# Performance work log

Measured on AMD Instinct MI355X. Metric: run time of the kernel, lower is better.

Reference implementation:

```python
import jax, jax.numpy as jnp
import numpy as np
import math

N = 2048; L = 100; D_IN = 128; D_STATE = 16; D_INNER = 256
MAMBA_DIM = 128; GAT_HID = 64; HEADS = 4; GAT_OUT = 64


def _lin(key, fin, fout, scale=0.02):
    k1, k2 = jax.random.split(key)
    return (jax.random.normal(k1, (fin, fout), jnp.float32) * scale,
            jnp.zeros((fout,), jnp.float32))


def setup_inputs() -> dict:
    key = jax.random.key(0)
    ks = jax.random.split(key, 16)
    temporal_data = jax.random.normal(ks[0], (N, L, D_IN), jnp.float32)
    graph_x = jax.random.normal(ks[1], (N, D_IN), jnp.float32)
    adj = (jax.random.uniform(ks[2], (N, N)) < 0.005).astype(jnp.float32)
    adj_matrix = jnp.maximum(adj, jnp.eye(N, dtype=jnp.float32))
    pos_emb = jax.random.normal(ks[3], (1, 100, D_IN), jnp.float32)
    Wi, bi = _lin(ks[4], D_IN, D_INNER)
    Wg, bg = _lin(ks[5], D_IN, D_INNER)
    A_log = jnp.linspace(math.log(1e-3), math.log(0.1), D_STATE).reshape(1, D_STATE).astype(jnp.float32)
    Wb, bb = _lin(ks[6], D_INNER, D_STATE)
    Wc, bc = _lin(ks[7], D_IN, D_STATE)
    Wo, bo = _lin(ks[8], D_INNER, D_IN)
    Wfc, bfc = _lin(ks[9], D_IN, MAMBA_DIM)
    W1 = jax.random.normal(ks[10], (HEADS, D_IN, GAT_HID), jnp.float32) * 0.05
    a1 = jax.random.normal(ks[11], (HEADS, 2 * GAT_HID), jnp.float32) * 0.05
    W2 = jax.random.normal(ks[12], (1, HEADS * GAT_HID, GAT_OUT), jnp.float32) * 0.05
    a2 = jax.random.normal(ks[13], (1, 2 * GAT_OUT), jnp.float32) * 0.05
    return dict(temporal_data=temporal_data, graph_x=graph_x, adj_matrix=adj_matrix,
                pos_emb=pos_emb, Wi=Wi, bi=bi, Wg=Wg, bg=bg, A_log=A_log,
                Wb=Wb, bb=bb, Wc=Wc, bc=bc, Wo=Wo, bo=bo, Wfc=Wfc, bfc=bfc,
                W1=W1, a1=a1, W2=W2, a2=a2)


def _mamba(x, pos_emb, Wi, bi, Wg, bg, A_log, Wb, bb, Wc, bc, Wo, bo):
    Bt, Ls, _ = x.shape
    x = x + pos_emb[:, :Ls, :]
    x_gated = (x @ Wi + bi) * jax.nn.sigmoid(x @ Wg + bg)   # [B,L,d_inner]
    Bmat = x_gated @ Wb + bb                                 # [B,L,d_state]
    Cmat = x @ Wc + bc                                       # [B,L,d_state]
    A = jnp.exp(0.01 * jnp.exp(A_log))                       # [1,d_state] (dt=0.01)

    def step(h, bc):
        b, c = bc
        h = A * h + b
        return h, h * c

    h0 = jnp.zeros((Bt, A_log.shape[1]), x.dtype)
    _, ys = jax.lax.scan(step, h0, (jnp.swapaxes(Bmat, 0, 1), jnp.swapaxes(Cmat, 0, 1)))
    y = jnp.swapaxes(ys, 0, 1)                               # [B,L,d_state]
    d_inner = Wo.shape[0]
    out_exp = jnp.concatenate(
        [y, jnp.zeros((Bt, Ls, d_inner - y.shape[-1]), x.dtype)], axis=-1)
    return out_exp @ Wo + bo


def _gat_layer(x, adj, W, a, concat):
    # x: [N,Fin], W: [H,Fin,Fout], a: [H,2*Fout]
    F_out = W.shape[2]
    xt = jnp.einsum('nf,hfo->hno', x, W)                     # [H,N,Fout]
    e_src = jnp.einsum('hno,ho->hn', xt, a[:, :F_out])       # a . x_i part
    e_dst = jnp.einsum('hno,ho->hn', xt, a[:, F_out:])       # a . x_j part
    e = jax.nn.leaky_relu(e_src[:, :, None] + e_dst[:, None, :], 0.2)
    e = jnp.where(adj[None, :, :] > 0, e, -jnp.inf)
    att = jax.nn.softmax(e, axis=2)                          # masked entries -> 0
    h_prime = jnp.einsum('hij,hjo->hio', att, xt)            # [H,N,Fout]
    if concat:
        return jnp.transpose(h_prime, (1, 0, 2)).reshape(x.shape[0], -1)
    return h_prime.mean(axis=0)


def reference(temporal_data, graph_x, adj_matrix, pos_emb, Wi, bi, Wg, bg, A_log,
              Wb, bb, Wc, bc, Wo, bo, Wfc, bfc, W1, a1, W2, a2):
    mamba_out = _mamba(temporal_data, pos_emb, Wi, bi, Wg, bg, A_log, Wb, bb, Wc, bc, Wo, bo)
    mamba_features = mamba_out @ Wfc + bfc
    # GAT stack (dropout is identity in eval mode)
    h = _gat_layer(graph_x, adj_matrix, W1, a1, concat=True)
    h = jax.nn.relu(h)
    gat_features = _gat_layer(h, adj_matrix, W2, a2, concat=False)
    return mamba_features, gat_features
```

## Files before the change

### kernel.cpp

```cpp
#include <hip/hip_runtime.h>
#include <hip/hip_bf16.h>

#define N_NODES 2048
#define L_SEQ   100
#define ROWS    (N_NODES * L_SEQ)
#define HEADS   4
#define GHID    64

typedef __attribute__((ext_vector_type(8))) short bf16x8;
typedef __attribute__((ext_vector_type(4))) float floatx4;

__device__ __forceinline__ short f2bf(float f) {
    union { float f; unsigned u; } v; v.f = f;
    return (short)((v.u + 0x8000u) >> 16);
}

constexpr size_t OFF_WCOMB = 0;
constexpr size_t OFF_BCOMB = 2048;
constexpr size_t OFF_AEXP  = 2176;
constexpr size_t OFF_WIGS  = 2192;
constexpr size_t OFF_WBS   = 34960;
constexpr size_t OFF_WCS   = 37008;
constexpr size_t OFF_BM    = 38032;
constexpr size_t OFF_CM    = OFF_BM + (size_t)ROWS * 16;
constexpr size_t OFF_XT1   = OFF_BM;
constexpr size_t OFF_ES1   = OFF_XT1 + (size_t)HEADS * N_NODES * GHID;
constexpr size_t OFF_ED1   = OFF_ES1 + HEADS * N_NODES;
constexpr size_t OFF_H1    = OFF_ED1 + HEADS * N_NODES;
constexpr size_t OFF_XT2   = OFF_H1 + (size_t)N_NODES * 256;
constexpr size_t OFF_ES2   = OFF_XT2 + (size_t)N_NODES * 64;
constexpr size_t OFF_ED2   = OFF_ES2 + N_NODES;

__global__ __launch_bounds__(256) void kA_prep(
    const float* __restrict__ Wo, const float* __restrict__ bo,
    const float* __restrict__ Wfc, const float* __restrict__ bfc,
    const float* __restrict__ A_log,
    const float* __restrict__ Wi, const float* __restrict__ Wg,
    const float* __restrict__ Wb, const float* __restrict__ Wc,
    float* __restrict__ ws) {
    const int b = blockIdx.x;
    if (b < 9) {
        int i = b * 256 + threadIdx.x;
        if (i < 2048) {
            int row = i >> 7, col = i & 127;
            float a = 0.f;
            for (int f = 0; f < 128; f++) a += Wo[row * 128 + f] * Wfc[f * 128 + col];
            ws[OFF_WCOMB + i] = a;
        } else if (i < 2176) {
            int col = i - 2048;
            float acc = bfc[col];
            for (int f = 0; f < 128; f++) acc += bo[f] * Wfc[f * 128 + col];
            ws[OFF_BCOMB + col] = acc;
        } else if (i < 2192) {
            int s = i - 2176;
            ws[OFF_AEXP + s] = expf(0.01f * expf(A_log[s]));
        }
        return;
    }
    int i = (b - 9) * 256 + threadIdx.x;
    short* wigs = (short*)(ws + OFF_WIGS);
    short* wbs  = (short*)(ws + OFF_WBS);
    short* wcs  = (short*)(ws + OFF_WCS);
    if (i < 65536) {
        int j = i & 7, lane = (i >> 3) & 63, ks = (i >> 9) & 3, nt = i >> 11;
        int w = nt >> 3, t = nt & 7;
        int col = w * 64 + (t & 3) * 16 + (lane & 15);
        int k   = ks * 32 + (lane >> 4) * 8 + j;
        float v = (t < 4) ? Wi[k * 256 + col] : Wg[k * 256 + col];
        wigs[i] = f2bf(v);
    } else if (i < 65536 + 4096) {
        int ii = i - 65536;
        int j = ii & 7, lane = (ii >> 3) & 63, ks = ii >> 9;
        int k = ks * 32 + (lane >> 4) * 8 + j, n = lane & 15;
        wbs[ii] = f2bf(Wb[k * 16 + n]);
    } else if (i < 65536 + 4096 + 2048) {
        int ii = i - 65536 - 4096;
        int j = ii & 7, lane = (ii >> 3) & 63, ks = ii >> 9;
        int k = ks * 32 + (lane >> 4) * 8 + j, n = lane & 15;
        wcs[ii] = f2bf(Wc[k * 16 + n]);
    }
}

__global__ __launch_bounds__(512, 4) void k1_mfma(
    const float* __restrict__ temporal, const float* __restrict__ pos,
    const float* __restrict__ bi, const float* __restrict__ bg,
    const float* __restrict__ bb, const float* __restrict__ bc,
    const float* __restrict__ ws, float* __restrict__ Bm, float* __restrict__ Cm) {
    __shared__ short xbf[64][136];
    __shared__ short gbf[64][264];
    const int tid = threadIdx.x, wave = tid >> 6, lane = tid & 63;
    const int m = lane & 15, quad = lane >> 4;
    const int r0 = blockIdx.x * 64;
    const int l0 = r0 % L_SEQ;

#pragma unroll
    for (int i = 0; i < 4; i++) {
        int f4  = i * 512 + tid;
        int row = f4 >> 5;
        int c4  = (f4 & 31) * 4;
        int l = l0 + row; if (l >= L_SEQ) l -= L_SEQ;
        float4 tv = *(const float4*)(temporal + (size_t)(r0 + row) * 128 + c4);
        float4 pv = *(const float4*)(pos + l * 128 + c4);
        short4 sv;
        sv.x = f2bf(tv.x + pv.x); sv.y = f2bf(tv.y + pv.y);
        sv.z = f2bf(tv.z + pv.z); sv.w = f2bf(tv.w + pv.w);
        *(short4*)&xbf[row][c4] = sv;
    }
    __syncthreads();

    const short* Wigs = (const short*)(ws + OFF_WIGS);
    const int wg = wave >> 1, wp = wave & 1;
    floatx4 acc[4][4] = {};
#pragma unroll
    for (int ks = 0; ks < 4; ks++) {
        bf16x8 bfr[4];
#pragma unroll
        for (int jl = 0; jl < 4; jl++) {
            int ntg = wg * 8 + wp * 2 + (jl & 1) + ((jl >> 1) << 2);
            bfr[jl] = *(const bf16x8*)(Wigs + (size_t)((ntg * 4 + ks) * 64 + lane) * 8);
        }
        bf16x8 afr[4];
#pragma unroll
        for (int mt = 0; mt < 4; mt++)
            afr[mt] = *(const bf16x8*)&xbf[mt * 16 + m][ks * 32 + quad * 8];
#pragma unroll
        for (int mt = 0; mt < 4; mt++)
#pragma unroll
            for (int jl = 0; jl < 4; jl++)
                acc[mt][jl] = __builtin_amdgcn_mfma_f32_16x16x32_bf16(
                    afr[mt], bfr[jl], acc[mt][jl], 0, 0, 0);
    }

    const float NL2E = -1.44269504f;
#pragma unroll
    for (int tp = 0; tp < 2; tp++) {
        int col = wave * 32 + tp * 16 + m;
        float biv = bi[col];
        float bgs = bg[col] * NL2E;
#pragma unroll
        for (int mt = 0; mt < 4; mt++) {
#pragma unroll
            for (int r = 0; r < 4; r++) {
                float li = acc[mt][tp][r] + biv;
                float ex = __builtin_amdgcn_exp2f(fmaf(acc[mt][tp + 2][r], NL2E, bgs));
                float g  = li * __builtin_amdgcn_rcpf(1.f + ex);
                gbf[mt * 16 + quad * 4 + r][col] = f2bf(g);
            }
        }
    }
    __syncthreads();

    if (wave < 4) {
        const short* Wbs = (const short*)(ws + OFF_WBS);
        floatx4 accB = {};
#pragma unroll
        for (int ks = 0; ks < 8; ks++) {
            bf16x8 a = *(const bf16x8*)&gbf[wave * 16 + m][ks * 32 + quad * 8];
            bf16x8 b = *(const bf16x8*)(Wbs + (size_t)(ks * 64 + lane) * 8);
            accB = __builtin_amdgcn_mfma_f32_16x16x32_bf16(a, b, accB, 0, 0, 0);
        }
        float bbv = bb[m];
#pragma unroll
        for (int r = 0; r < 4; r++) {
            int row = r0 + wave * 16 + quad * 4 + r;
            Bm[(size_t)row * 16 + m] = accB[r] + bbv;
        }
    } else {
        const short* Wcs = (const short*)(ws + OFF_WCS);
        const int mt = wave - 4;
        floatx4 accC = {};
#pragma unroll
        for (int ks = 0; ks < 4; ks++) {
            bf16x8 a = *(const bf16x8*)&xbf[mt * 16 + m][ks * 32 + quad * 8];
            bf16x8 b = *(const bf16x8*)(Wcs + (size_t)(ks * 64 + lane) * 8);
            accC = __builtin_amdgcn_mfma_f32_16x16x32_bf16(a, b, accC, 0, 0, 0);
        }
        float bcv = bc[m];
#pragma unroll
        for (int r = 0; r < 4; r++) {
            int row = r0 + mt * 16 + quad * 4 + r;
            Cm[(size_t)row * 16 + m] = accC[r] + bcv;
        }
    }
}

__global__ __launch_bounds__(256) void k2_scan(const float* __restrict__ ws,
                                               float* __restrict__ out) {
    __shared__ float sb[2][1600], sc[2][1600];
    const int sub = threadIdx.x >> 7, f = threadIdx.x & 127;
    const int n = blockIdx.x * 2 + sub;
    const float4* Bm4 = (const float4*)(ws + OFF_BM + (size_t)n * 1600);
    const float4* Cm4 = (const float4*)(ws + OFF_CM + (size_t)n * 1600);
#pragma unroll
    for (int i = 0; i < 4; i++) {
        int idx = i * 128 + f;
        if (idx < 400) {
            ((float4*)sb[sub])[idx] = Bm4[idx];
            ((float4*)sc[sub])[idx] = Cm4[idx];
        }
    }
    float w[16], A[16], h[16];
#pragma unroll
    for (int s = 0; s < 16; s++) {
        w[s] = ws[OFF_WCOMB + s * 128 + f];
        A[s] = ws[OFF_AEXP + s];
        h[s] = 0.f;
    }
    const float bcb = ws[OFF_BCOMB + f];
    __syncthreads();
    const float* sbn = sb[sub];
    const float* scn = sc[sub];
    for (int l = 0; l < L_SEQ; l++) {
        float acc0 = bcb, acc1 = 0.f;
#pragma unroll
        for (int s = 0; s < 8; s++) {
            h[s] = A[s] * h[s] + sbn[l * 16 + s];
            acc0 += h[s] * scn[l * 16 + s] * w[s];
        }
#pragma unroll
        for (int s = 8; s < 16; s++) {
            h[s] = A[s] * h[s] + sbn[l * 16 + s];
            acc1 += h[s] * scn[l * 16 + s] * w[s];
        }
        out[((size_t)n * L_SEQ + l) * 128 + f] = acc0 + acc1;
    }
}

__global__ __launch_bounds__(256) void k4_xt1(const float* __restrict__ gx,
                                              const float* __restrict__ W1,
                                              const float* __restrict__ a1,
                                              float* __restrict__ ws) {
    const int n = blockIdx.x;
    const int h = threadIdx.x >> 6, o = threadIdx.x & 63;
    float acc = 0.f;
    for (int f = 0; f < 128; f++)
        acc += gx[n * 128 + f] * W1[(h * 128 + f) * 64 + o];
    ws[OFF_XT1 + ((size_t)h * 2048 + n) * 64 + o] = acc;
    float es = acc * a1[h * 128 + o];
    float ed = acc * a1[h * 128 + 64 + o];
#pragma unroll
    for (int off = 32; off > 0; off >>= 1) {
        es += __shfl_down(es, off);
        ed += __shfl_down(ed, off);
    }
    if (o == 0) { ws[OFF_ES1 + h * 2048 + n] = es; ws[OFF_ED1 + h * 2048 + n] = ed; }
}

__global__ __launch_bounds__(256) void k56_att1(const float* __restrict__ adj,
                                                const float* __restrict__ W2,
                                                const float* __restrict__ a2,
                                                float* __restrict__ ws) {
    __shared__ int list[2048];
    __shared__ int cnt;
    __shared__ float sh1[256];
    __shared__ float sred[4][64];
    const int n = blockIdx.x, tid = threadIdx.x;
    if (tid == 0) cnt = 0;
    __syncthreads();
    for (int j = tid; j < 2048; j += 256)
        if (adj[(size_t)n * 2048 + j] > 0.f) list[atomicAdd(&cnt, 1)] = j;
    __syncthreads();
    const int h = tid >> 6, o = tid & 63;
    {
        const float  es = ws[OFF_ES1 + h * 2048 + n];
        const float* ed = ws + OFF_ED1 + h * 2048;
        const float* xt = ws + OFF_XT1 + (size_t)h * 2048 * 64;
        float num = 0.f, den = 0.f;
        const int mm = cnt;
        for (int ii = 0; ii < mm; ii++) {
            int j = list[ii];
            float e = es + ed[j];
            e = (e > 0.f) ? e : 0.2f * e;
            float wgt = expf(e);
            den += wgt;
            num += wgt * xt[(size_t)j * 64 + o];
        }
        float v = num / den;
        sh1[h * 64 + o] = v > 0.f ? v : 0.f;
    }
    __syncthreads();
    {
        const int g = h, o2 = o;
        float part = 0.f;
        const int f0 = g * 64;
#pragma unroll 8
        for (int f = 0; f < 64; f++)
            part += sh1[f0 + f] * W2[(f0 + f) * 64 + o2];
        sred[g][o2] = part;
    }
    __syncthreads();
    if (tid < 64) {
        float xt2v = sred[0][tid] + sred[1][tid] + sred[2][tid] + sred[3][tid];
        ws[OFF_XT2 + (size_t)n * 64 + tid] = xt2v;
        float es = xt2v * a2[tid];
        float ed = xt2v * a2[64 + tid];
#pragma unroll
        for (int off = 32; off > 0; off >>= 1) {
            es += __shfl_down(es, off);
            ed += __shfl_down(ed, off);
        }
        if (tid == 0) { ws[OFF_ES2 + n] = es; ws[OFF_ED2 + n] = ed; }
    }
}

__global__ __launch_bounds__(256) void k7_att2(const float* __restrict__ adj,
                                               const float* __restrict__ ws,
                                               float* __restrict__ gout) {
    __shared__ int list[2048];
    __shared__ int cnt;
    __shared__ float snum[4][64];
    __shared__ float sden[4];
    const int n = blockIdx.x, tid = threadIdx.x;
    const int g = tid >> 6, o = tid & 63;
    if (tid == 0) cnt = 0;
    __syncthreads();
    for (int j = tid; j < 2048; j += 256)
        if (adj[(size_t)n * 2048 + j] > 0.f) list[atomicAdd(&cnt, 1)] = j;
    __syncthreads();
    const float es = ws[OFF_ES2 + n];
    float num = 0.f, den = 0.f;
    const int mm = cnt;
    for (int ii = g; ii < mm; ii += 4) {
        int j = list[ii];
        float e = es + ws[OFF_ED2 + j];
        e = (e > 0.f) ? e : 0.2f * e;
        float wgt = expf(e);
        den += wgt;
        num += wgt * ws[OFF_XT2 + (size_t)j * 64 + o];
    }
    snum[g][o] = num;
    if (o == 0) sden[g] = den;
    __syncthreads();
    if (tid < 64) {
        float nt = snum[0][tid] + snum[1][tid] + snum[2][tid] + snum[3][tid];
        float dt = sden[0] + sden[1] + sden[2] + sden[3];
        gout[(size_t)n * 64 + tid] = nt / dt;
    }
}

extern "C" void kernel_launch(void* const* d_in, const int* in_sizes, int n_in,
                              void* d_out, int out_size, void* d_ws, size_t ws_size,
                              hipStream_t stream) {
    const float* temporal = (const float*)d_in[0];
    const float* graph_x  = (const float*)d_in[1];
    const float* adj      = (const float*)d_in[2];
    const float* pos      = (const float*)d_in[3];
    const float* Wi  = (const float*)d_in[4];
    const float* bi  = (const float*)d_in[5];
    const float* Wg  = (const float*)d_in[6];
    const float* bg  = (const float*)d_in[7];
    const float* A_log = (const float*)d_in[8];
    const float* Wb  = (const float*)d_in[9];
    const float* bb  = (const float*)d_in[10];
    const float* Wc  = (const float*)d_in[11];
    const float* bc  = (const float*)d_in[12];
    const float* Wo  = (const float*)d_in[13];
    const float* bo  = (const float*)d_in[14];
    const float* Wfc = (const float*)d_in[15];
    const float* bfc = (const float*)d_in[16];
    const float* W1  = (const float*)d_in[17];
    const float* a1  = (const float*)d_in[18];
    const float* W2  = (const float*)d_in[19];
    const float* a2  = (const float*)d_in[20];

    float* ws = (float*)d_ws;
    float* out_mamba = (float*)d_out;
    float* out_gat   = out_mamba + (size_t)ROWS * 128;

    kA_prep<<<289, 256, 0, stream>>>(Wo, bo, Wfc, bfc, A_log, Wi, Wg, Wb, Wc, ws);
    k1_mfma<<<ROWS / 64, 512, 0, stream>>>(temporal, pos, bi, bg, bb, bc, ws,
                                           ws + OFF_BM, ws + OFF_CM);
    k2_scan<<<N_NODES / 2, 256, 0, stream>>>(ws, out_mamba);
    k4_xt1<<<N_NODES, 256, 0, stream>>>(graph_x, W1, a1, ws);
    k56_att1<<<N_NODES, 256, 0, stream>>>(adj, W2, a2, ws);
    k7_att2<<<N_NODES, 256, 0, stream>>>(adj, ws, out_gat);
}
```

Baseline: 327.9 us.

## Fuse scan and GAT stages into one cooperative kernel with grid syncs

The scan, GAT xt1, attention-1 and attention-2 stages are merged into a single cooperative kernel of 1024 blocks, each handling two nodes, separated by grid.sync. If the cooperative launch fails, the code falls back to four separate launches. The scan is also restructured: 16 threads run the recurrence per state and write h*C into shared memory, then all threads do the output projection with float4 reads. This removes launch gaps but serialises the recurrence onto 16 lanes per node, and it adds grid-barrier cost plus a co-residency requirement for the cooperative launch.

After: 975.9 us. 2.98x slower.

```diff
diff --git a/kernel.cpp b/kernel.cpp
--- a/kernel.cpp
+++ b/kernel.cpp
@@ -1,5 +1,8 @@
 #include <hip/hip_runtime.h>
 #include <hip/hip_bf16.h>
+#include <hip/hip_cooperative_groups.h>
+
+namespace cg = cooperative_groups;
 
 #define N_NODES 2048
 #define L_SEQ   100
@@ -184,158 +187,209 @@
     }
 }
 
-__global__ __launch_bounds__(256) void k2_scan(const float* __restrict__ ws,
-                                               float* __restrict__ out) {
-    __shared__ float sb[2][1600], sc[2][1600];
-    const int sub = threadIdx.x >> 7, f = threadIdx.x & 127;
-    const int n = blockIdx.x * 2 + sub;
-    const float4* Bm4 = (const float4*)(ws + OFF_BM + (size_t)n * 1600);
-    const float4* Cm4 = (const float4*)(ws + OFF_CM + (size_t)n * 1600);
-#pragma unroll
-    for (int i = 0; i < 4; i++) {
-        int idx = i * 128 + f;
-        if (idx < 400) {
-            ((float4*)sb[sub])[idx] = Bm4[idx];
-            ((float4*)sc[sub])[idx] = Cm4[idx];
-        }
-    }
-    float w[16], A[16], h[16];
-#pragma unroll
-    for (int s = 0; s < 16; s++) {
-        w[s] = ws[OFF_WCOMB + s * 128 + f];
-        A[s] = ws[OFF_AEXP + s];
-        h[s] = 0.f;
-    }
-    const float bcb = ws[OFF_BCOMB + f];
+
+union GatSmem {
+    float ys[2][1600];
+    struct { int list[2048]; int cnt; float sh1[256]; float sred[4][64]; } c;
+    struct { int list[2048]; int cnt; float snum[4][64]; float sden[4]; } d;
+};
+
+__device__ __forceinline__ void phaseA_scan(const float* ws, float* out,
+                                            GatSmem& sm, int bid) {
+    const int tid = threadIdx.x;
+    const int sub = tid >> 7, t = tid & 127;
+    const int n = bid * 2 + sub;
+    float w[16];
+#pragma unroll
+    for (int s = 0; s < 16; s++) w[s] = ws[OFF_WCOMB + s * 128 + t];
+    const float bcb = ws[OFF_BCOMB + t];
+    if (t < 16) {
+        const int s = t;
+        const float As = ws[OFF_AEXP + s];
+        const float* bmp = ws + OFF_BM + (size_t)n * 1600 + s;
+        const float* cmp = ws + OFF_CM + (size_t)n * 1600 + s;
+        float h = 0.f;
+#pragma unroll
+        for (int lc = 0; lc < 4; lc++) {
+            float lb[25], lv[25];
+#pragma unroll
+            for (int q = 0; q < 25; q++) {
+                lb[q] = bmp[(lc * 25 + q) * 16];
+                lv[q] = cmp[(lc * 25 + q) * 16];
+            }
+#pragma unroll
+            for (int q = 0; q < 25; q++) {
+                h = As * h + lb[q];
+                sm.ys[sub][(lc * 25 + q) * 16 + s] = h * lv[q];
+            }
+        }
+    }
     __syncthreads();
-    const float* sbn = sb[sub];
-    const float* scn = sc[sub];
+    const float* ysn = sm.ys[sub];
+    float* op = out + (size_t)n * L_SEQ * 128 + t;
+#pragma unroll 2
     for (int l = 0; l < L_SEQ; l++) {
-        float acc0 = bcb, acc1 = 0.f;
-#pragma unroll
-        for (int s = 0; s < 8; s++) {
-            h[s] = A[s] * h[s] + sbn[l * 16 + s];
-            acc0 += h[s] * scn[l * 16 + s] * w[s];
-        }
-#pragma unroll
-        for (int s = 8; s < 16; s++) {
-            h[s] = A[s] * h[s] + sbn[l * 16 + s];
-            acc1 += h[s] * scn[l * 16 + s] * w[s];
-        }
-        out[((size_t)n * L_SEQ + l) * 128 + f] = acc0 + acc1;
-    }
-}
-
-__global__ __launch_bounds__(256) void k4_xt1(const float* __restrict__ gx,
-                                              const float* __restrict__ W1,
-                                              const float* __restrict__ a1,
-                                              float* __restrict__ ws) {
-    const int n = blockIdx.x;
-    const int h = threadIdx.x >> 6, o = threadIdx.x & 63;
-    float acc = 0.f;
-    for (int f = 0; f < 128; f++)
-        acc += gx[n * 128 + f] * W1[(h * 128 + f) * 64 + o];
-    ws[OFF_XT1 + ((size_t)h * 2048 + n) * 64 + o] = acc;
-    float es = acc * a1[h * 128 + o];
-    float ed = acc * a1[h * 128 + 64 + o];
-#pragma unroll
-    for (int off = 32; off > 0; off >>= 1) {
-        es += __shfl_down(es, off);
-        ed += __shfl_down(ed, off);
-    }
-    if (o == 0) { ws[OFF_ES1 + h * 2048 + n] = es; ws[OFF_ED1 + h * 2048 + n] = ed; }
-}
-
-__global__ __launch_bounds__(256) void k56_att1(const float* __restrict__ adj,
-                                                const float* __restrict__ W2,
-                                                const float* __restrict__ a2,
-                                                float* __restrict__ ws) {
-    __shared__ int list[2048];
-    __shared__ int cnt;
-    __shared__ float sh1[256];
-    __shared__ float sred[4][64];
-    const int n = blockIdx.x, tid = threadIdx.x;
-    if (tid == 0) cnt = 0;
-    __syncthreads();
-    for (int j = tid; j < 2048; j += 256)
-        if (adj[(size_t)n * 2048 + j] > 0.f) list[atomicAdd(&cnt, 1)] = j;
-    __syncthreads();
+        const float4 y0 = *(const float4*)(ysn + l * 16 + 0);
+        const float4 y1 = *(const float4*)(ysn + l * 16 + 4);
+        const float4 y2 = *(const float4*)(ysn + l * 16 + 8);
+        const float4 y3 = *(const float4*)(ysn + l * 16 + 12);
+        float a0 = fmaf(y0.x, w[0], bcb);
+        float a1 = y0.y * w[1];
+        float a2 = y0.z * w[2];
+        float a3 = y0.w * w[3];
+        a0 = fmaf(y1.x, w[4], a0); a1 = fmaf(y1.y, w[5], a1);
+        a2 = fmaf(y1.z, w[6], a2); a3 = fmaf(y1.w, w[7], a3);
+        a0 = fmaf(y2.x, w[8], a0); a1 = fmaf(y2.y, w[9], a1);
+        a2 = fmaf(y2.z, w[10], a2); a3 = fmaf(y2.w, w[11], a3);
+        a0 = fmaf(y3.x, w[12], a0); a1 = fmaf(y3.y, w[13], a1);
+        a2 = fmaf(y3.z, w[14], a2); a3 = fmaf(y3.w, w[15], a3);
+        op[(size_t)l * 128] = (a0 + a1) + (a2 + a3);
+    }
+}
+
+__device__ __forceinline__ void phaseB_xt1(const float* gx, const float* W1,
+                                           const float* a1, float* ws, int bid) {
+    const int tid = threadIdx.x;
     const int h = tid >> 6, o = tid & 63;
-    {
-        const float  es = ws[OFF_ES1 + h * 2048 + n];
-        const float* ed = ws + OFF_ED1 + h * 2048;
-        const float* xt = ws + OFF_XT1 + (size_t)h * 2048 * 64;
+    for (int nn = 0; nn < 2; nn++) {
+        const int n = bid * 2 + nn;
+        float acc = 0.f;
+        for (int f = 0; f < 128; f++)
+            acc += gx[n * 128 + f] * W1[(h * 128 + f) * 64 + o];
+        ws[OFF_XT1 + ((size_t)h * 2048 + n) * 64 + o] = acc;
+        float es = acc * a1[h * 128 + o];
+        float ed = acc * a1[h * 128 + 64 + o];
+#pragma unroll
+        for (int off = 32; off > 0; off >>= 1) {
+            es += __shfl_down(es, off);
+            ed += __shfl_down(ed, off);
+        }
+        if (o == 0) { ws[OFF_ES1 + h * 2048 + n] = es; ws[OFF_ED1 + h * 2048 + n] = ed; }
+    }
+}
+
+__device__ __forceinline__ void phaseC_att1(const float* adj, const float* W2,
+                                            const float* a2, float* ws,
+                                            GatSmem& sm, int bid) {
+    const int tid = threadIdx.x;
+    const int h = tid >> 6, o = tid & 63;
+    for (int nn = 0; nn < 2; nn++) {
+        const int n = bid * 2 + nn;
+        __syncthreads();
+        if (tid == 0) sm.c.cnt = 0;
+        __syncthreads();
+        for (int j = tid; j < 2048; j += 256)
+            if (adj[(size_t)n * 2048 + j] > 0.f) sm.c.list[atomicAdd(&sm.c.cnt, 1)] = j;
+        __syncthreads();
+        {
+            const float  es = ws[OFF_ES1 + h * 2048 + n];
+            const float* ed = ws + OFF_ED1 + h * 2048;
+            const float* xt = ws + OFF_XT1 + (size_t)h * 2048 * 64;
+            float num = 0.f, den = 0.f;
+            const int mm = sm.c.cnt;
+            for (int ii = 0; ii < mm; ii++) {
+                int j = sm.c.list[ii];
+                float e = es + ed[j];
+                e = (e > 0.f) ? e : 0.2f * e;
+                float wgt = expf(e);
+                den += wgt;
+                num += wgt * xt[(size_t)j * 64 + o];
+            }
+            float v = num / den;
+            sm.c.sh1[h * 64 + o] = v > 0.f ? v : 0.f;
+        }
+        __syncthreads();
+        {
+            float part = 0.f;
+            const int f0 = h * 64;
+#pragma unroll 8
+            for (int f = 0; f < 64; f++)
+                part += sm.c.sh1[f0 + f] * W2[(f0 + f) * 64 + o];
+            sm.c.sred[h][o] = part;
+        }
+        __syncthreads();
+        if (tid < 64) {
+            float xt2v = sm.c.sred[0][tid] + sm.c.sred[1][tid]
+                       + sm.c.sred[2][tid] + sm.c.sred[3][tid];
+            ws[OFF_XT2 + (size_t)n * 64 + tid] = xt2v;
+            float es = xt2v * a2[tid];
+            float ed = xt2v * a2[64 + tid];
+#pragma unroll
+            for (int off = 32; off > 0; off >>= 1) {
+                es += __shfl_down(es, off);
+                ed += __shfl_down(ed, off);
+            }
+            if (tid == 0) { ws[OFF_ES2 + n] = es; ws[OFF_ED2 + n] = ed; }
+        }
+    }
+}
+
+__device__ __forceinline__ void phaseD_att2(const float* adj, const float* ws,
+                                            float* gout, GatSmem& sm, int bid) {
+    const int tid = threadIdx.x;
+    const int g = tid >> 6, o = tid & 63;
+    for (int nn = 0; nn < 2; nn++) {
+        const int n = bid * 2 + nn;
+        __syncthreads();
+        if (tid == 0) sm.d.cnt = 0;
+        __syncthreads();
+        for (int j = tid; j < 2048; j += 256)
+            if (adj[(size_t)n * 2048 + j] > 0.f) sm.d.list[atomicAdd(&sm.d.cnt, 1)] = j;
+        __syncthreads();
+        const float es = ws[OFF_ES2 + n];
         float num = 0.f, den = 0.f;
-        const int mm = cnt;
-        for (int ii = 0; ii < mm; ii++) {
-            int j = list[ii];
-            float e = es + ed[j];
+        const int mm = sm.d.cnt;
+        for (int ii = g; ii < mm; ii += 4) {
+            int j = sm.d.list[ii];
+            float e = es + ws[OFF_ED2 + j];
             e = (e > 0.f) ? e : 0.2f * e;
             float wgt = expf(e);
             den += wgt;
-            num += wgt * xt[(size_t)j * 64 + o];
-        }
-        float v = num / den;
-        sh1[h * 64 + o] = v > 0.f ? v : 0.f;
-    }
-    __syncthreads();
-    {
-        const int g = h, o2 = o;
-        float part = 0.f;
-        const int f0 = g * 64;
-#pragma unroll 8
-        for (int f = 0; f < 64; f++)
-            part += sh1[f0 + f] * W2[(f0 + f) * 64 + o2];
-        sred[g][o2] = part;
-    }
-    __syncthreads();
-    if (tid < 64) {
-        float xt2v = sred[0][tid] + sred[1][tid] + sred[2][tid] + sred[3][tid];
-        ws[OFF_XT2 + (size_t)n * 64 + tid] = xt2v;
-        float es = xt2v * a2[tid];
-        float ed = xt2v * a2[64 + tid];
-#pragma unroll
-        for (int off = 32; off > 0; off >>= 1) {
-            es += __shfl_down(es, off);
-            ed += __shfl_down(ed, off);
-        }
-        if (tid == 0) { ws[OFF_ES2 + n] = es; ws[OFF_ED2 + n] = ed; }
-    }
-}
-
-__global__ __launch_bounds__(256) void k7_att2(const float* __restrict__ adj,
-                                               const float* __restrict__ ws,
-                                               float* __restrict__ gout) {
-    __shared__ int list[2048];
-    __shared__ int cnt;
-    __shared__ float snum[4][64];
-    __shared__ float sden[4];
-    const int n = blockIdx.x, tid = threadIdx.x;
-    const int g = tid >> 6, o = tid & 63;
-    if (tid == 0) cnt = 0;
-    __syncthreads();
-    for (int j = tid; j < 2048; j += 256)
-        if (adj[(size_t)n * 2048 + j] > 0.f) list[atomicAdd(&cnt, 1)] = j;
-    __syncthreads();
-    const float es = ws[OFF_ES2 + n];
-    float num = 0.f, den = 0.f;
-    const int mm = cnt;
-    for (int ii = g; ii < mm; ii += 4) {
-        int j = list[ii];
-        float e = es + ws[OFF_ED2 + j];
-        e = (e > 0.f) ? e : 0.2f * e;
-        float wgt = expf(e);
-        den += wgt;
-        num += wgt * ws[OFF_XT2 + (size_t)j * 64 + o];
-    }
-    snum[g][o] = num;
-    if (o == 0) sden[g] = den;
-    __syncthreads();
-    if (tid < 64) {
-        float nt = snum[0][tid] + snum[1][tid] + snum[2][tid] + snum[3][tid];
-        float dt = sden[0] + sden[1] + sden[2] + sden[3];
-        gout[(size_t)n * 64 + tid] = nt / dt;
-    }
+            num += wgt * ws[OFF_XT2 + (size_t)j * 64 + o];
+        }
+        sm.d.snum[g][o] = num;
+        if (o == 0) sm.d.sden[g] = den;
+        __syncthreads();
+        if (tid < 64) {
+            float nt = sm.d.snum[0][tid] + sm.d.snum[1][tid]
+                     + sm.d.snum[2][tid] + sm.d.snum[3][tid];
+            float dt = sm.d.sden[0] + sm.d.sden[1] + sm.d.sden[2] + sm.d.sden[3];
+            gout[(size_t)n * 64 + tid] = nt / dt;
+        }
+    }
+}
+
+__global__ __launch_bounds__(256) void kMega(
+    const float* adj, const float* gx, const float* W1, const float* a1,
+    const float* W2, const float* a2, float* ws, float* outm, float* outg) {
+    __shared__ GatSmem sm;
+    cg::grid_group grid = cg::this_grid();
+    phaseA_scan(ws, outm, sm, blockIdx.x);
+    __threadfence(); grid.sync();
+    phaseB_xt1(gx, W1, a1, ws, blockIdx.x);
+    __threadfence(); grid.sync();
+    phaseC_att1(adj, W2, a2, ws, sm, blockIdx.x);
+    __threadfence(); grid.sync();
+    phaseD_att2(adj, ws, outg, sm, blockIdx.x);
+}
+
+__global__ __launch_bounds__(256) void kP_scan(const float* ws, float* out) {
+    __shared__ GatSmem sm;
+    phaseA_scan(ws, out, sm, blockIdx.x);
+}
+__global__ __launch_bounds__(256) void kP_xt1(const float* gx, const float* W1,
+                                              const float* a1, float* ws) {
+    phaseB_xt1(gx, W1, a1, ws, blockIdx.x);
+}
+__global__ __launch_bounds__(256) void kP_att1(const float* adj, const float* W2,
+                                               const float* a2, float* ws) {
+    __shared__ GatSmem sm;
+    phaseC_att1(adj, W2, a2, ws, sm, blockIdx.x);
+}
+__global__ __launch_bounds__(256) void kP_att2(const float* adj, const float* ws,
+                                               float* gout) {
+    __shared__ GatSmem sm;
+    phaseD_att2(adj, ws, gout, sm, blockIdx.x);
 }
 
 extern "C" void kernel_launch(void* const* d_in, const int* in_sizes, int n_in,
@@ -370,8 +424,17 @@
     kA_prep<<<289, 256, 0, stream>>>(Wo, bo, Wfc, bfc, A_log, Wi, Wg, Wb, Wc, ws);
     k1_mfma<<<ROWS / 64, 512, 0, stream>>>(temporal, pos, bi, bg, bb, bc, ws,
                                            ws + OFF_BM, ws + OFF_CM);
-    k2_scan<<<N_NODES / 2, 256, 0, stream>>>(ws, out_mamba);
-    k4_xt1<<<N_NODES, 256, 0, stream>>>(graph_x, W1, a1, ws);
-    k56_att1<<<N_NODES, 256, 0, stream>>>(adj, W2, a2, ws);
-    k7_att2<<<N_NODES, 256, 0, stream>>>(adj, ws, out_gat);
-}
+
+    void* args[] = { (void*)&adj, (void*)&graph_x, (void*)&W1, (void*)&a1,
+                     (void*)&W2, (void*)&a2, (void*)&ws,
+                     (void*)&out_mamba, (void*)&out_gat };
+    hipError_t ce = hipLaunchCooperativeKernel((const void*)kMega, dim3(1024),
+                                               dim3(256), args, 0, stream);
+    if (ce != hipSuccess) {
+        (void)hipGetLastError();
+        kP_scan<<<1024, 256, 0, stream>>>(ws, out_mamba);
+        kP_xt1<<<1024, 256, 0, stream>>>(graph_x, W1, a1, ws);
+        kP_att1<<<1024, 256, 0, stream>>>(adj, W2, a2, ws);
+        kP_att2<<<1024, 256, 0, stream>>>(adj, ws, out_gat);
+    }
+}
```

## Precompute scan states once per node and fuse scan with GAT projection

Applied to the files above, without the earlier changes.

The scan is restructured so 16 threads compute the recurrence h*C per state once per node and store it in shared memory. All 128 output channels then read those values as float4 and do only a 16-term dot product, instead of every channel thread recomputing the full recurrence. The GAT xt1 projection is merged into the same launch as extra blocks when the workspace is large enough, which needs a relocated GAT workspace region. The serial 16-thread phase leaves most of the block idle, and the fused path depends on the workspace size.

Result: no change. 327.4 us (-0.1%).

```diff
diff --git a/kernel.cpp b/kernel.cpp
--- a/kernel.cpp
+++ b/kernel.cpp
@@ -23,13 +23,15 @@
 constexpr size_t OFF_WCS   = 37008;
 constexpr size_t OFF_BM    = 38032;
 constexpr size_t OFF_CM    = OFF_BM + (size_t)ROWS * 16;
-constexpr size_t OFF_XT1   = OFF_BM;
-constexpr size_t OFF_ES1   = OFF_XT1 + (size_t)HEADS * N_NODES * GHID;
-constexpr size_t OFF_ED1   = OFF_ES1 + HEADS * N_NODES;
-constexpr size_t OFF_H1    = OFF_ED1 + HEADS * N_NODES;
-constexpr size_t OFF_XT2   = OFF_H1 + (size_t)N_NODES * 256;
-constexpr size_t OFF_ES2   = OFF_XT2 + (size_t)N_NODES * 64;
-constexpr size_t OFF_ED2   = OFF_ES2 + N_NODES;
+constexpr size_t OFF_GAT_BIG = OFF_CM + (size_t)ROWS * 16;
+
+constexpr size_t GXT1 = 0;
+constexpr size_t GES1 = (size_t)HEADS * N_NODES * GHID;
+constexpr size_t GED1 = GES1 + (size_t)HEADS * N_NODES;
+constexpr size_t GXT2 = GED1 + (size_t)HEADS * N_NODES;
+constexpr size_t GES2 = GXT2 + (size_t)N_NODES * GHID;
+constexpr size_t GED2 = GES2 + N_NODES;
+constexpr size_t GAT_TOTAL = GED2 + N_NODES;
 
 __global__ __launch_bounds__(256) void kA_prep(
     const float* __restrict__ Wo, const float* __restrict__ bo,
@@ -184,72 +186,118 @@
     }
 }
 
+struct __align__(16) ScanSmem { float sb[2][1600]; float sc[2][1600]; };
+
+__device__ __forceinline__ void scan_body(const float* __restrict__ ws,
+                                          float* __restrict__ out,
+                                          ScanSmem& sm, int bid) {
+    const int tid = threadIdx.x;
+    const int sub = tid >> 7, t = tid & 127;
+    const int n = bid * 2 + sub;
+    float* sbp = sm.sb[sub];
+    float* scp = sm.sc[sub];
+    const float4* Bm4 = (const float4*)(ws + OFF_BM + (size_t)n * 1600);
+    const float4* Cm4 = (const float4*)(ws + OFF_CM + (size_t)n * 1600);
+#pragma unroll
+    for (int i = 0; i < 4; i++) {
+        int idx = i * 128 + t;
+        if (idx < 400) {
+            ((float4*)sbp)[idx] = Bm4[idx];
+            ((float4*)scp)[idx] = Cm4[idx];
+        }
+    }
+    float w[16];
+#pragma unroll
+    for (int s = 0; s < 16; s++) w[s] = ws[OFF_WCOMB + s * 128 + t];
+    const float bcb = ws[OFF_BCOMB + t];
+    __syncthreads();
+    if (t < 16) {
+        const int s = t;
+        const float As = ws[OFF_AEXP + s];
+        float h = 0.f;
+#pragma unroll
+        for (int lc = 0; lc < 5; lc++) {
+            float lb[20], lv[20];
+#pragma unroll
+            for (int q = 0; q < 20; q++) {
+                lb[q] = sbp[(lc * 20 + q) * 16 + s];
+                lv[q] = scp[(lc * 20 + q) * 16 + s];
+            }
+#pragma unroll
+            for (int q = 0; q < 20; q++) {
+                h = fmaf(As, h, lb[q]);
+                sbp[(lc * 20 + q) * 16 + s] = h * lv[q];
+            }
+        }
+    }
+    __syncthreads();
+    float* op = out + (size_t)n * L_SEQ * 128 + t;
+#pragma unroll 2
+    for (int l = 0; l < L_SEQ; l++) {
+        const float4 y0 = *(const float4*)(sbp + l * 16 + 0);
+        const float4 y1 = *(const float4*)(sbp + l * 16 + 4);
+        const float4 y2 = *(const float4*)(sbp + l * 16 + 8);
+        const float4 y3 = *(const float4*)(sbp + l * 16 + 12);
+        float a0 = fmaf(y0.x, w[0], bcb);
+        float a1 = y0.y * w[1];
+        float a2 = y0.z * w[2];
+        float a3 = y0.w * w[3];
+        a0 = fmaf(y1.x, w[4], a0); a1 = fmaf(y1.y, w[5], a1);
+        a2 = fmaf(y1.z, w[6], a2); a3 = fmaf(y1.w, w[7], a3);
+        a0 = fmaf(y2.x, w[8], a0); a1 = fmaf(y2.y, w[9], a1);
+        a2 = fmaf(y2.z, w[10], a2); a3 = fmaf(y2.w, w[11], a3);
+        a0 = fmaf(y3.x, w[12], a0); a1 = fmaf(y3.y, w[13], a1);
+        a2 = fmaf(y3.z, w[14], a2); a3 = fmaf(y3.w, w[15], a3);
+        op[(size_t)l * 128] = (a0 + a1) + (a2 + a3);
+    }
+}
+
+__device__ __forceinline__ void xt1_body(const float* __restrict__ gx,
+                                         const float* __restrict__ W1,
+                                         const float* __restrict__ a1,
+                                         float* __restrict__ gat, int n) {
+    const int tid = threadIdx.x;
+    const int h = tid >> 6, o = tid & 63;
+    float acc = 0.f;
+    for (int f = 0; f < 128; f++)
+        acc += gx[n * 128 + f] * W1[(h * 128 + f) * 64 + o];
+    gat[GXT1 + ((size_t)h * 2048 + n) * 64 + o] = acc;
+    float es = acc * a1[h * 128 + o];
+    float ed = acc * a1[h * 128 + 64 + o];
+#pragma unroll
+    for (int off = 32; off > 0; off >>= 1) {
+        es += __shfl_down(es, off);
+        ed += __shfl_down(ed, off);
+    }
+    if (o == 0) { gat[GES1 + h * 2048 + n] = es; gat[GED1 + h * 2048 + n] = ed; }
+}
+
 __global__ __launch_bounds__(256) void k2_scan(const float* __restrict__ ws,
                                                float* __restrict__ out) {
-    __shared__ float sb[2][1600], sc[2][1600];
-    const int sub = threadIdx.x >> 7, f = threadIdx.x & 127;
-    const int n = blockIdx.x * 2 + sub;
-    const float4* Bm4 = (const float4*)(ws + OFF_BM + (size_t)n * 1600);
-    const float4* Cm4 = (const float4*)(ws + OFF_CM + (size_t)n * 1600);
-#pragma unroll
-    for (int i = 0; i < 4; i++) {
-        int idx = i * 128 + f;
-        if (idx < 400) {
-            ((float4*)sb[sub])[idx] = Bm4[idx];
-            ((float4*)sc[sub])[idx] = Cm4[idx];
-        }
-    }
-    float w[16], A[16], h[16];
-#pragma unroll
-    for (int s = 0; s < 16; s++) {
-        w[s] = ws[OFF_WCOMB + s * 128 + f];
-        A[s] = ws[OFF_AEXP + s];
-        h[s] = 0.f;
-    }
-    const float bcb = ws[OFF_BCOMB + f];
-    __syncthreads();
-    const float* sbn = sb[sub];
-    const float* scn = sc[sub];
-    for (int l = 0; l < L_SEQ; l++) {
-        float acc0 = bcb, acc1 = 0.f;
-#pragma unroll
-        for (int s = 0; s < 8; s++) {
-            h[s] = A[s] * h[s] + sbn[l * 16 + s];
-            acc0 += h[s] * scn[l * 16 + s] * w[s];
-        }
-#pragma unroll
-        for (int s = 8; s < 16; s++) {
-            h[s] = A[s] * h[s] + sbn[l * 16 + s];
-            acc1 += h[s] * scn[l * 16 + s] * w[s];
-        }
-        out[((size_t)n * L_SEQ + l) * 128 + f] = acc0 + acc1;
-    }
+    __shared__ ScanSmem sm;
+    scan_body(ws, out, sm, blockIdx.x);
 }
 
 __global__ __launch_bounds__(256) void k4_xt1(const float* __restrict__ gx,
                                               const float* __restrict__ W1,
                                               const float* __restrict__ a1,
-                                              float* __restrict__ ws) {
-    const int n = blockIdx.x;
-    const int h = threadIdx.x >> 6, o = threadIdx.x & 63;
-    float acc = 0.f;
-    for (int f = 0; f < 128; f++)
-        acc += gx[n * 128 + f] * W1[(h * 128 + f) * 64 + o];
-    ws[OFF_XT1 + ((size_t)h * 2048 + n) * 64 + o] = acc;
-    float es = acc * a1[h * 128 + o];
-    float ed = acc * a1[h * 128 + 64 + o];
-#pragma unroll
-    for (int off = 32; off > 0; off >>= 1) {
-        es += __shfl_down(es, off);
-        ed += __shfl_down(ed, off);
-    }
-    if (o == 0) { ws[OFF_ES1 + h * 2048 + n] = es; ws[OFF_ED1 + h * 2048 + n] = ed; }
+                                              float* __restrict__ gat) {
+    xt1_body(gx, W1, a1, gat, blockIdx.x);
+}
+
+__global__ __launch_bounds__(256) void k24_fused(
+    const float* __restrict__ ws, float* __restrict__ out,
+    const float* __restrict__ gx, const float* __restrict__ W1,
+    const float* __restrict__ a1, float* __restrict__ gat) {
+    __shared__ ScanSmem sm;
+    if (blockIdx.x < N_NODES / 2) scan_body(ws, out, sm, blockIdx.x);
+    else                          xt1_body(gx, W1, a1, gat, blockIdx.x - N_NODES / 2);
 }
 
 __global__ __launch_bounds__(256) void k56_att1(const float* __restrict__ adj,
                                                 const float* __restrict__ W2,
                                                 const float* __restrict__ a2,
-                                                float* __restrict__ ws) {
+                                                float* __restrict__ gat) {
     __shared__ int list[2048];
     __shared__ int cnt;
     __shared__ float sh1[256];
@@ -262,9 +310,9 @@
     __syncthreads();
     const int h = tid >> 6, o = tid & 63;
     {
-        const float  es = ws[OFF_ES1 + h * 2048 + n];
-        const float* ed = ws + OFF_ED1 + h * 2048;
-        const float* xt = ws + OFF_XT1 + (size_t)h * 2048 * 64;
+        const float  es = gat[GES1 + h * 2048 + n];
+        const float* ed = gat + GED1 + h * 2048;
+        const float* xt = gat + GXT1 + (size_t)h * 2048 * 64;
         float num = 0.f, den = 0.f;
         const int mm = cnt;
         for (int ii = 0; ii < mm; ii++) {
@@ -280,18 +328,17 @@
     }
     __syncthreads();
     {
-        const int g = h, o2 = o;
         float part = 0.f;
-        const int f0 = g * 64;
+        const int f0 = h * 64;
 #pragma unroll 8
         for (int f = 0; f < 64; f++)
-            part += sh1[f0 + f] * W2[(f0 + f) * 64 + o2];
-        sred[g][o2] = part;
+            part += sh1[f0 + f] * W2[(f0 + f) * 64 + o];
+        sred[h][o] = part;
     }
     __syncthreads();
     if (tid < 64) {
         float xt2v = sred[0][tid] + sred[1][tid] + sred[2][tid] + sred[3][tid];
-        ws[OFF_XT2 + (size_t)n * 64 + tid] = xt2v;
+        gat[GXT2 + (size_t)n * 64 + tid] = xt2v;
         float es = xt2v * a2[tid];
         float ed = xt2v * a2[64 + tid];
 #pragma unroll
@@ -299,12 +346,12 @@
             es += __shfl_down(es, off);
             ed += __shfl_down(ed, off);
         }
-        if (tid == 0) { ws[OFF_ES2 + n] = es; ws[OFF_ED2 + n] = ed; }
+        if (tid == 0) { gat[GES2 + n] = es; gat[GED2 + n] = ed; }
     }
 }
 
 __global__ __launch_bounds__(256) void k7_att2(const float* __restrict__ adj,
-                                               const float* __restrict__ ws,
+                                               const float* __restrict__ gat,
                                                float* __restrict__ gout) {
     __shared__ int list[2048];
     __shared__ int cnt;
@@ -317,16 +364,16 @@
     for (int j = tid; j < 2048; j += 256)
         if (adj[(size_t)n * 2048 + j] > 0.f) list[atomicAdd(&cnt, 1)] = j;
     __syncthreads();
-    const float es = ws[OFF_ES2 + n];
+    const float es = gat[GES2 + n];
     float num = 0.f, den = 0.f;
     const int mm = cnt;
     for (int ii = g; ii < mm; ii += 4) {
         int j = list[ii];
-        float e = es + ws[OFF_ED2 + j];
+        float e = es + gat[GED2 + j];
         e = (e > 0.f) ? e : 0.2f * e;
         float wgt = expf(e);
         den += wgt;
-        num += wgt * ws[OFF_XT2 + (size_t)j * 64 + o];
+        num += wgt * gat[GXT2 + (size_t)j * 64 + o];
     }
     snum[g][o] = num;
     if (o == 0) sden[g] = den;
@@ -367,11 +414,19 @@
     float* out_mamba = (float*)d_out;
     float* out_gat   = out_mamba + (size_t)ROWS * 128;
 
+    const bool big_ws = ws_size >= (OFF_GAT_BIG + GAT_TOTAL) * sizeof(float);
+    float* gat = big_ws ? (ws + OFF_GAT_BIG) : (ws + OFF_BM);
+
     kA_prep<<<289, 256, 0, stream>>>(Wo, bo, Wfc, bfc, A_log, Wi, Wg, Wb, Wc, ws);
     k1_mfma<<<ROWS / 64, 512, 0, stream>>>(temporal, pos, bi, bg, bb, bc, ws,
                                            ws + OFF_BM, ws + OFF_CM);
-    k2_scan<<<N_NODES / 2, 256, 0, stream>>>(ws, out_mamba);
-    k4_xt1<<<N_NODES, 256, 0, stream>>>(graph_x, W1, a1, ws);
-    k56_att1<<<N_NODES, 256, 0, stream>>>(adj, W2, a2, ws);
-    k7_att2<<<N_NODES, 256, 0, stream>>>(adj, ws, out_gat);
-}
+    if (big_ws) {
+        k24_fused<<<N_NODES / 2 + N_NODES, 256, 0, stream>>>(ws, out_mamba,
+                                                             graph_x, W1, a1, gat);
+    } else {
+        k2_scan<<<N_NODES / 2, 256, 0, stream>>>(ws, out_mamba);
+        k4_xt1<<<N_NODES, 256, 0, stream>>>(graph_x, W1, a1, gat);
+    }
+    k56_att1<<<N_NODES, 256, 0, stream>>>(adj, W2, a2, gat);
+    k7_att2<<<N_NODES, 256, 0, stream>>>(adj, gat, out_gat);
+}
```
